# Kernel optimization log

Hardware: AMD Instinct MI355X
Metric: run time of the kernel (lower is better)

## Reference

```python
import jax, jax.numpy as jnp
import numpy as np

N = 256        # SSM state size
D_MODEL = 2048 # number of independent channels sharing the kernel
L_MAX = 4096   # sequence length


def setup_inputs() -> dict:
    key = jax.random.key(0)
    k1, k2, k3, k4 = jax.random.split(key, 4)
    s = float(np.sqrt(N))
    # Stable A: eigenvalues with negative real part so A^l stays bounded after
    # bilinear discretization with step = 1/L.
    A = 0.5 * jax.random.normal(k1, (N, N), jnp.float32) / s - jnp.eye(N, dtype=jnp.float32)
    B = jax.random.normal(k2, (N, 1), jnp.float32) / s   # lecun-scale
    C = jax.random.normal(k3, (1, N), jnp.float32) / s
    D = jnp.ones((1,), jnp.float32)
    y = jax.random.normal(k4, (D_MODEL, L_MAX), jnp.float32)
    return {"y": y, "A": A, "B": B, "C": C, "D": D}


def _build_kernel(A, B, C, L, step):
    # Bilinear (Tustin) discretization, as in discretize_SSM.
    I = jnp.eye(A.shape[0], dtype=A.dtype)
    BL = jnp.linalg.inv(I - (step / 2.0) * A)
    Abar = BL @ (I + (step / 2.0) * A)
    Bbar = (BL * step) @ B                      # (N, 1)
    # K[l] = C @ Abar^l @ Bbar, computed as L matvecs via scan
    # (same math as the matrix_power loop, without O(L*N^3) cost).
    def step_fn(x, _):
        return Abar @ x, (C @ x)[0]
    _, K = jax.lax.scan(step_fn, Bbar[:, 0], None, length=L)
    return K                                     # (L,)


def _causal_conv(y, K):
    # mode='full' convolution truncated to first L samples == causal conv.
    L = y.shape[-1]
    n = 2 * L
    Yf = jnp.fft.rfft(y, n=n, axis=-1)           # (d_model, n//2+1)
    Kf = jnp.fft.rfft(K, n=n)                    # (n//2+1,)
    return jnp.fft.irfft(Yf * Kf, n=n, axis=-1)[..., :L]


def reference(y, A, B, C, D):
    L = y.shape[-1]
    K = _build_kernel(A, B, C, L, step=1.0 / L)
    return _causal_conv(y, K) + D * y
```

## Files before the change

kernel.cpp:

```cpp
#include <hip/hip_runtime.h>

#define N_ 256
#define L_ 4096
#define DM_ 2048
#define STEPF (1.0f / 4096.0f)
#define NW 15
#define NV 6
#define RQN 4608

typedef short bf16x8 __attribute__((ext_vector_type(8)));
typedef float f32x4 __attribute__((ext_vector_type(4)));
typedef unsigned int uint32;

__device__ __forceinline__ uint32 bf16rne(float f) {
    uint32 u = __builtin_bit_cast(uint32, f);
    return (u + 0x7FFFu + ((u >> 16) & 1u)) >> 16;
}
__device__ __forceinline__ float rdlane(float v, int l) {
    return __builtin_bit_cast(float, __builtin_amdgcn_readlane(__builtin_bit_cast(int, v), l));
}

__global__ __launch_bounds__(1024) void k_kry(const float* __restrict__ Araw,
                                              const float* __restrict__ Bv,
                                              const float* __restrict__ Cv,
                                              float* __restrict__ W,
                                              float* __restrict__ V) {
    __shared__ float kry[NW][256];
    __shared__ float red[4][256];
    __shared__ float cur[256];
    const int tid = threadIdx.x;
    const int j = tid & 255, seg = tid >> 8, lane = tid & 63;

#define DOT64(S0, S1, VV) { \
    _Pragma("unroll") \
    for (int m = 0; m < 64; m += 2) { \
        S0 = fmaf(rdlane(VV, m), a[m], S0); \
        S1 = fmaf(rdlane(VV, m + 1), a[m + 1], S1); \
    } }

    if (blockIdx.x == 0) {
        float a[64];
#pragma unroll
        for (int m = 0; m < 64; ++m) a[m] = Araw[(64 * seg + m) * 256 + j];
        if (tid < 256) kry[0][tid] = Cv[tid];
        __syncthreads();
        const float WSC = 4032.0f / 4096.0f;
        for (int n = 1; n < NW; ++n) {
            float vv = kry[n - 1][64 * seg + lane];
            float s0 = 0.f, s1 = 0.f;
            DOT64(s0, s1, vv)
            red[seg][j] = s0 + s1;
            __syncthreads();
            if (tid < 256)
                kry[n][tid] = (red[0][tid] + red[1][tid] + red[2][tid] + red[3][tid]) * (WSC / (float)n);
            __syncthreads();
        }
        float kj[NW];
#pragma unroll
        for (int n = 0; n < NW; ++n) kj[n] = kry[n][j];
        for (int u = 0; u < 16; ++u) {
            int q = seg + 4 * u;
            float c = (float)q * (1.0f / 63.0f);
            float h = kj[NW - 1];
#pragma unroll
            for (int n = NW - 2; n >= 0; --n) h = fmaf(c, h, kj[n]);
            W[q * 256 + j] = h;
        }
    } else {
        float a[64];
#pragma unroll
        for (int m = 0; m < 64; ++m) a[m] = Araw[j * 256 + 64 * seg + m];
        if (tid < 256) cur[tid] = Bv[tid];
        __syncthreads();
        const float ms = 0.5f * STEPF;
        for (int it = 0; it < 3; ++it) {
            float vv = cur[64 * seg + lane];
            float s0 = 0.f, s1 = 0.f;
            DOT64(s0, s1, vv)
            red[seg][j] = s0 + s1;
            __syncthreads();
            if (tid < 256)
                cur[tid] = fmaf(ms, red[0][tid] + red[1][tid] + red[2][tid] + red[3][tid], Bv[tid]);
            __syncthreads();
        }
        if (tid < 256) kry[0][tid] = STEPF * cur[tid];
        __syncthreads();
        const float VSC = 63.0f / 4096.0f;
        for (int n = 1; n < NV; ++n) {
            float vv = kry[n - 1][64 * seg + lane];
            float s0 = 0.f, s1 = 0.f;
            DOT64(s0, s1, vv)
            red[seg][j] = s0 + s1;
            __syncthreads();
            if (tid < 256)
                kry[n][tid] = (red[0][tid] + red[1][tid] + red[2][tid] + red[3][tid]) * (VSC / (float)n);
            __syncthreads();
        }
        float kj[NV];
#pragma unroll
        for (int n = 0; n < NV; ++n) kj[n] = kry[n][j];
        for (int u = 0; u < 16; ++u) {
            int r = seg + 4 * u;
            float c = (float)r * (1.0f / 63.0f);
            float h = kj[NV - 1];
#pragma unroll
            for (int n = NV - 2; n >= 0; --n) h = fmaf(c, h, kj[n]);
            V[j * 64 + r] = h;
        }
    }
#undef DOT64
}

__global__ __launch_bounds__(256) void k_g(const float* __restrict__ A, const float* __restrict__ B,
                                           float* __restrict__ C, int Ma, int Nb,
                                           int lda, int ldb, int ldc, float alpha, float diagv) {
    int row0 = blockIdx.y * 32, col0 = blockIdx.x * 32;
    if (row0 >= Ma || col0 >= Nb) return;
    __shared__ float As[16][33], Bs[16][33];
    int tid = threadIdx.x;
    int tx = tid & 15, ty = tid >> 4;
    int e0 = tid * 2, e1 = e0 + 1;
    int ai0 = e0 >> 4, ak0 = e0 & 15, ai1 = e1 >> 4, ak1 = e1 & 15;
    int bj0 = e0 & 31, bk0 = e0 >> 5, bj1 = e1 & 31, bk1 = e1 >> 5;
    bool va0 = (row0 + ai0) < Ma, va1 = (row0 + ai1) < Ma;
    bool vb0 = (col0 + bj0) < Nb, vb1 = (col0 + bj1) < Nb;
    float a0p = va0 ? A[(row0 + ai0) * lda + ak0] : 0.f;
    float a1p = va1 ? A[(row0 + ai1) * lda + ak1] : 0.f;
    float b0p = vb0 ? B[bk0 * ldb + col0 + bj0] : 0.f;
    float b1p = vb1 ? B[bk1 * ldb + col0 + bj1] : 0.f;
    float acc00 = 0.f, acc01 = 0.f, acc10 = 0.f, acc11 = 0.f;
    for (int kk = 0; kk < 256; kk += 16) {
        As[ak0][ai0] = a0p; As[ak1][ai1] = a1p;
        Bs[bk0][bj0] = b0p; Bs[bk1][bj1] = b1p;
        __syncthreads();
        if (kk + 16 < 256) {
            a0p = va0 ? A[(row0 + ai0) * lda + kk + 16 + ak0] : 0.f;
            a1p = va1 ? A[(row0 + ai1) * lda + kk + 16 + ak1] : 0.f;
            b0p = vb0 ? B[(bk0 + kk + 16) * ldb + col0 + bj0] : 0.f;
            b1p = vb1 ? B[(bk1 + kk + 16) * ldb + col0 + bj1] : 0.f;
        }
#pragma unroll
        for (int k = 0; k < 16; ++k) {
            float a0 = As[k][ty * 2], a1 = As[k][ty * 2 + 1];
            float b0 = Bs[k][tx * 2], b1 = Bs[k][tx * 2 + 1];
            acc00 = fmaf(a0, b0, acc00); acc01 = fmaf(a0, b1, acc01);
            acc10 = fmaf(a1, b0, acc10); acc11 = fmaf(a1, b1, acc11);
        }
        __syncthreads();
    }
    float accs[2][2] = {{acc00, acc01}, {acc10, acc11}};
#pragma unroll
    for (int i = 0; i < 2; ++i) {
        int r = row0 + ty * 2 + i;
        if (r < Ma)
#pragma unroll
            for (int jj = 0; jj < 2; ++jj) {
                int c = col0 + tx * 2 + jj;
                if (c < Nb) {
                    float v = alpha * accs[i][jj];
                    if (r == c) v += diagv;
                    C[r * ldc + c] = v;
                }
            }
    }
}

__global__ __launch_bounds__(256) void k_pack(const float* __restrict__ Kf, uint2* __restrict__ Rqg) {
    int i = blockIdx.x * 256 + threadIdx.x;
    int a = 4095 - i;
    uint32 e0 = (a >= 0) ? bf16rne(Kf[a]) : 0u;
    uint32 e1 = (a >= 1) ? bf16rne(Kf[a - 1]) : 0u;
    uint32 e2 = (a >= 2) ? bf16rne(Kf[a - 2]) : 0u;
    uint32 e3 = (a >= 3) ? bf16rne(Kf[a - 3]) : 0u;
    uint2 v; v.x = e0 | (e1 << 16); v.y = e2 | (e3 << 16);
    Rqg[i] = v;
}

__global__ __launch_bounds__(256, 2) void k_conv(const uint2* __restrict__ Rqg,
                                                 const float* __restrict__ y,
                                                 const float* __restrict__ Dp,
                                                 float* __restrict__ out) {
    __shared__ uint2 Rq[RQN];
    const int tid = threadIdx.x;
#pragma unroll
    for (int i = 0; i < RQN / 256; ++i) Rq[i * 256 + tid] = Rqg[i * 256 + tid];
    __syncthreads();

    const int w = tid >> 6, lane = tid & 63;
    const int n = lane & 15, g = lane >> 4;
    const int by = (int)blockIdx.y;
    const int d0w = (int)blockIdx.x * 64 + w * 16;
    const int d = d0w + n;
    const float4* __restrict__ yq = (const float4*)(y + (size_t)d * L_);
    const float D0 = Dp[0];

#define LOADF(SL, I0) { \
    uint2 u0 = Rq[(I0)]; uint2 u1 = Rq[(I0) + 4]; \
    uint4 uu; uu.x = u0.x; uu.y = u0.y; uu.z = u1.x; uu.w = u1.y; \
    fr[SL] = __builtin_bit_cast(bf16x8, uu); }
#define PK2(LO, HI) __builtin_amdgcn_perm(__builtin_bit_cast(uint32, (HI)), \
                                          __builtin_bit_cast(uint32, (LO)), 0x07060302u)
#define PACKAV(Q0, Q1) { \
    uint4 ua; ua.x = PK2((Q0).x, (Q0).y); ua.y = PK2((Q0).z, (Q0).w); \
    ua.z = PK2((Q1).x, (Q1).y); ua.w = PK2((Q1).z, (Q1).w); \
    av = __builtin_bit_cast(bf16x8, ua); }
#define MF(TI, SL) acc[TI] = __builtin_amdgcn_mfma_f32_16x16x32_bf16(av, fr[SL], acc[TI], 0, 0, 0);

#define STEPB(YI, S0,S1,S2,S3,S4,S5,S6,S7,S8,S9,S10,S11,S12,S13,S14,S15) { \
    PACKAV(q0a, q0b); \
    q0a = q1a; q0b = q1b; \
    __builtin_amdgcn_s_setprio(1); \
    MF(14, S14) MF(15, S15) \
    LOADF(S14, bcur + 32) LOADF(S15, bcur + 16) \
    q1a = yq[(YI)]; q1b = yq[(YI) + 1]; \
    yn += 8; bcur += 32; \
    MF(0,S0) MF(1,S1) MF(2,S2) MF(3,S3) MF(4,S4) MF(5,S5) MF(6,S6) MF(7,S7) \
    MF(8,S8) MF(9,S9) MF(10,S10) MF(11,S11) MF(12,S12) MF(13,S13) \
    __builtin_amdgcn_s_setprio(0); \
}

#define ROUND8(YIM) \
    STEPB(YIM, 0,1,2,3,4,5,6,7,8,9,10,11,12,13,14,15) \
    STEPB(YIM, 14,15,0,1,2,3,4,5,6,7,8,9,10,11,12,13) \
    STEPB(YIM, 12,13,14,15,0,1,2,3,4,5,6,7,8,9,10,11) \
    STEPB(YIM, 10,11,12,13,14,15,0,1,2,3,4,5,6,7,8,9) \
    STEPB(YIM, 8,9,10,11,12,13,14,15,0,1,2,3,4,5,6,7) \
    STEPB(YIM, 6,7,8,9,10,11,12,13,14,15,0,1,2,3,4,5) \
    STEPB(YIM, 4,5,6,7,8,9,10,11,12,13,14,15,0,1,2,3) \
    STEPB(YIM, 2,3,4,5,6,7,8,9,10,11,12,13,14,15,0,1)

    for (int strip = 0; strip < 2; ++strip) {
        const int v = strip ? by : (15 - by);
        const int t0 = v << 8;
        const int S = 8 * (v + 1);

        f32x4 acc[16];
#pragma unroll
        for (int i = 0; i < 16; ++i) acc[i] = (f32x4){0.f, 0.f, 0.f, 0.f};
        bf16x8 fr[16], av;
        float4 q0a, q0b, q1a, q1b;

        const int B0 = 4095 - t0 - n + 8 * g;
#pragma unroll
        for (int ti = 0; ti < 16; ++ti) LOADF(ti, B0 - 16 * ti)
        q0a = yq[2 * g];     q0b = yq[2 * g + 1];
        q1a = yq[8 + 2 * g]; q1b = yq[8 + 2 * g + 1];
        int bcur = B0;
        int yn = 16 + 2 * g;

        const int nfull = S >> 3;
        for (int it = 0; it < nfull - 1; ++it) {
            ROUND8(yn)
        }
        ROUND8(yn < 1016 ? yn : 1016)

#pragma unroll
        for (int ti = 0; ti < 16; ++ti) {
            int tcol = t0 + 16 * ti + n;
#pragma unroll
            for (int r = 0; r < 4; ++r) {
                int dr = d0w + 4 * g + r;
                size_t ix = (size_t)dr * L_ + tcol;
                out[ix] = acc[ti][r] + D0 * y[ix];
            }
        }
    }

#undef ROUND8
#undef STEPB
#undef MF
#undef PACKAV
#undef PK2
#undef LOADF
}


extern "C" void kernel_launch(void* const* d_in, const int* in_sizes, int n_in,
                              void* d_out, int out_size, void* d_ws, size_t ws_size,
                              hipStream_t stream) {
    const float* y  = (const float*)d_in[0];
    const float* A  = (const float*)d_in[1];
    const float* Bv = (const float*)d_in[2];
    const float* Cv = (const float*)d_in[3];
    const float* Dp = (const float*)d_in[4];
    float* out = (float*)d_out;
    float* w = (float*)d_ws;

    float* W   = w;
    float* V   = w + 16384;
    float* Kf  = w + 32768;
    uint2* Rqg = (uint2*)(w + 36864);

    k_kry<<<dim3(2), dim3(1024), 0, stream>>>(A, Bv, Cv, W, V);
    k_g<<<dim3(2, 2), dim3(256), 0, stream>>>(W, V, Kf, 64, 64, 256, 64, 64, 1.0f, 0.0f);
    k_pack<<<dim3(18), dim3(256), 0, stream>>>(Kf, Rqg);
    k_conv<<<dim3(32, 8), dim3(256), 0, stream>>>(Rqg, y, Dp, out);

    (void)in_sizes; (void)n_in; (void)out_size; (void)ws_size;
}
```

Baseline: 78.81 us.

## Split convolution reduction across wave pairs and double the block grid

```diff
diff --git a/kernel.cpp b/kernel.cpp
--- a/kernel.cpp
+++ b/kernel.cpp
@@ -181,6 +181,7 @@
                                                  const float* __restrict__ Dp,
                                                  float* __restrict__ out) {
     __shared__ uint2 Rq[RQN];
+    __shared__ f32x4 mbuf[2][8][64];
     const int tid = threadIdx.x;
 #pragma unroll
     for (int i = 0; i < RQN / 256; ++i) Rq[i * 256 + tid] = Rqg[i * 256 + tid];
@@ -188,8 +189,9 @@
 
     const int w = tid >> 6, lane = tid & 63;
     const int n = lane & 15, g = lane >> 4;
+    const int ds = w & 1, jh = w >> 1;
     const int by = (int)blockIdx.y;
-    const int d0w = (int)blockIdx.x * 64 + w * 16;
+    const int d0w = (int)blockIdx.x * 32 + ds * 16;
     const int d = d0w + n;
     const float4* __restrict__ yq = (const float4*)(y + (size_t)d * L_);
     const float D0 = Dp[0];
@@ -229,10 +231,17 @@
     STEPB(YIM, 4,5,6,7,8,9,10,11,12,13,14,15,0,1,2,3) \
     STEPB(YIM, 2,3,4,5,6,7,8,9,10,11,12,13,14,15,0,1)
 
+#define ROUND4(YIM) \
+    STEPB(YIM, 0,1,2,3,4,5,6,7,8,9,10,11,12,13,14,15) \
+    STEPB(YIM, 14,15,0,1,2,3,4,5,6,7,8,9,10,11,12,13) \
+    STEPB(YIM, 12,13,14,15,0,1,2,3,4,5,6,7,8,9,10,11) \
+    STEPB(YIM, 10,11,12,13,14,15,0,1,2,3,4,5,6,7,8,9)
+
     for (int strip = 0; strip < 2; ++strip) {
         const int v = strip ? by : (15 - by);
         const int t0 = v << 8;
-        const int S = 8 * (v + 1);
+        const int Sh = 4 * (v + 1);
+        const int s0 = jh * Sh;
 
         f32x4 acc[16];
 #pragma unroll
@@ -240,33 +249,58 @@
         bf16x8 fr[16], av;
         float4 q0a, q0b, q1a, q1b;
 
-        const int B0 = 4095 - t0 - n + 8 * g;
+        const int B0 = 4095 - t0 - n + 8 * g + 32 * s0;
 #pragma unroll
         for (int ti = 0; ti < 16; ++ti) LOADF(ti, B0 - 16 * ti)
-        q0a = yq[2 * g];     q0b = yq[2 * g + 1];
-        q1a = yq[8 + 2 * g]; q1b = yq[8 + 2 * g + 1];
+        q0a = yq[8 * s0 + 2 * g];     q0b = yq[8 * s0 + 2 * g + 1];
+        q1a = yq[8 * s0 + 8 + 2 * g]; q1b = yq[8 * s0 + 8 + 2 * g + 1];
         int bcur = B0;
-        int yn = 16 + 2 * g;
-
-        const int nfull = S >> 3;
-        for (int it = 0; it < nfull - 1; ++it) {
+        int yn = 8 * s0 + 16 + 2 * g;
+
+        const int n8 = Sh >> 3;
+        for (int it = 0; it < n8 - 1; ++it) {
             ROUND8(yn)
         }
-        ROUND8(yn < 1016 ? yn : 1016)
-
-#pragma unroll
-        for (int ti = 0; ti < 16; ++ti) {
-            int tcol = t0 + 16 * ti + n;
-#pragma unroll
-            for (int r = 0; r < 4; ++r) {
-                int dr = d0w + 4 * g + r;
-                size_t ix = (size_t)dr * L_ + tcol;
-                out[ix] = acc[ti][r] + D0 * y[ix];
+        if (n8 > 0) {
+            ROUND8(yn < 1016 ? yn : 1016)
+        }
+        if (Sh & 4) {
+            ROUND4(yn)
+        }
+
+#pragma unroll
+        for (int rr = 0; rr < 2; ++rr) {
+            if (jh == 1) {
+#pragma unroll
+                for (int i = 0; i < 8; ++i) mbuf[ds][i][lane] = acc[rr * 8 + i];
             }
+            __syncthreads();
+            if (jh == 0) {
+#pragma unroll
+                for (int i = 0; i < 8; ++i) {
+                    f32x4 m = mbuf[ds][i][lane];
+                    acc[rr * 8 + i][0] += m[0]; acc[rr * 8 + i][1] += m[1];
+                    acc[rr * 8 + i][2] += m[2]; acc[rr * 8 + i][3] += m[3];
+                }
+            }
+            __syncthreads();
+        }
+        if (jh == 0) {
+#pragma unroll
+            for (int ti = 0; ti < 16; ++ti) {
+                int tcol = t0 + 16 * ti + n;
+#pragma unroll
+                for (int r = 0; r < 4; ++r) {
+                    int dr = d0w + 4 * g + r;
+                    size_t ix = (size_t)dr * L_ + tcol;
+                    out[ix] = acc[ti][r] + D0 * y[ix];
+                }
+            }
         }
     }
 
 #undef ROUND8
+#undef ROUND4
 #undef STEPB
 #undef MF
 #undef PACKAV
@@ -294,7 +328,7 @@
     k_kry<<<dim3(2), dim3(1024), 0, stream>>>(A, Bv, Cv, W, V);
     k_g<<<dim3(2, 2), dim3(256), 0, stream>>>(W, V, Kf, 64, 64, 256, 64, 64, 1.0f, 0.0f);
     k_pack<<<dim3(18), dim3(256), 0, stream>>>(Kf, Rqg);
-    k_conv<<<dim3(32, 8), dim3(256), 0, stream>>>(Rqg, y, Dp, out);
+    k_conv<<<dim3(64, 8), dim3(256), 0, stream>>>(Rqg, y, Dp, out);
 
     (void)in_sizes; (void)n_in; (void)out_size; (void)ws_size;
 }
```

Result: no change. 80.27 us (+1.8%).
